# Kernel optimization log

Hardware: AMD Instinct MI355X
Metric: run time of the kernel (lower is better)

Reference implementation:

```python
import jax, jax.numpy as jnp
import numpy as np

N = 50000   # num nodes
E = 400000  # num edges (avg degree 8)
D = 256     # in_channels
H = 256     # hidden_channels
C = 64      # out_channels
K = 2       # k_hops


def setup_inputs() -> dict:
    key = jax.random.key(0)
    ks = jax.random.split(key, 10)
    x = jax.random.normal(ks[0], (N, D), dtype=jnp.float32)
    edge_index = jax.random.randint(ks[1], (2, E), 0, N, dtype=jnp.int32)
    s = 0.05
    # per-hop linears of the single H2GCNConv (weights stored [in, out])
    W0 = jax.random.normal(ks[2], (D, H), jnp.float32) * s
    W1 = jax.random.normal(ks[3], (D, H), jnp.float32) * s
    W2 = jax.random.normal(ks[4], (D, H), jnp.float32) * s
    b0 = jnp.zeros((H,), jnp.float32)
    b1 = jnp.zeros((H,), jnp.float32)
    b2 = jnp.zeros((H,), jnp.float32)
    # classifier: h2_out_dim = H*(K+1) = 768 -> C
    Wc = jax.random.normal(ks[5], (H * (K + 1), C), jnp.float32) * s
    bc = jnp.zeros((C,), jnp.float32)
    return {"x": x, "edge_index": edge_index, "num_nodes": N,
            "W0": W0, "b0": b0, "W1": W1, "b1": b1, "W2": W2, "b2": b2,
            "Wc": Wc, "bc": bc}


def _normalize_adj(edge_index, num_nodes):
    # add self loops, then D^{-1/2} A D^{-1/2} edge weights
    loops = jnp.arange(num_nodes, dtype=edge_index.dtype)
    ei = jnp.concatenate([edge_index, jnp.stack([loops, loops])], axis=1)
    row, col = ei[0], ei[1]
    deg = jax.ops.segment_sum(jnp.ones(row.shape[0], jnp.float32), row,
                              num_segments=num_nodes)
    dis = jnp.where(deg > 0, deg ** -0.5, 0.0)  # inf -> 0 for isolated nodes
    return ei, dis[row] * dis[col]


def _sparse_mm(edge_index, edge_weight, x, num_nodes):
    # gather -> scale -> scatter-add (COO SpMM)
    row, col = edge_index[0], edge_index[1]
    msg = x[col] * edge_weight[:, None]  # [E', F]
    return jax.ops.segment_sum(msg, row, num_segments=num_nodes)


def reference(x, edge_index, num_nodes, W0, b0, W1, b1, W2, b2, Wc, bc):
    ei, ew = _normalize_adj(edge_index, num_nodes)
    # H2GCNConv: ego + k-hop aggregates, each through its own linear, concat
    outs = [x @ W0 + b0]
    cur = x
    for Wk, bk in ((W1, b1), (W2, b2)):
        cur = _sparse_mm(ei, ew, cur, num_nodes)
        outs.append(cur @ Wk + bk)
    h = jax.nn.relu(jnp.concatenate(outs, axis=1))  # [N, 3H]
    # dropout p=0 / eval mode -> identity
    return h @ Wc + bc
```

## Files before the change

### kernel.cpp

```cpp
#include <hip/hip_runtime.h>


#define FD 256
#define CO 64
#define SB 512

using frag_ab = __attribute__((ext_vector_type(8))) short;
using f32x4   = __attribute__((ext_vector_type(4))) float;
typedef unsigned short u16;
typedef unsigned int   u32;

__device__ __forceinline__ u16 f2bf(float f) {
    u32 u = __builtin_bit_cast(u32, f);
    return (u16)((u + 0x7FFFu + ((u >> 16) & 1u)) >> 16);
}
__device__ __forceinline__ float bfl(u32 packed) {
    return __builtin_bit_cast(float, packed << 16);
}
__device__ __forceinline__ float bfh(u32 packed) {
    return __builtin_bit_cast(float, packed & 0xFFFF0000u);
}

__device__ __forceinline__ void gll16(const void* g, void* l) {
    __builtin_amdgcn_global_load_lds(
        (const __attribute__((address_space(1))) u32*)g,
        (__attribute__((address_space(3))) u32*)l, 16, 0, 0);
}

#define BAR()  __builtin_amdgcn_s_barrier()
#define WLG0() asm volatile("s_waitcnt lgkmcnt(0)" ::: "memory")
#define WVM0() asm volatile("s_waitcnt vmcnt(0)" ::: "memory")
#define WVM2() asm volatile("s_waitcnt vmcnt(2)" ::: "memory")

__global__ void zerok(int4* __restrict__ deg4, int4* __restrict__ fill4, int n4) {
    int i = blockIdx.x * blockDim.x + threadIdx.x;
    int4 z = make_int4(0, 0, 0, 0);
    if (i < n4) { deg4[i] = z; fill4[i] = z; }
}
__global__ void count_kernel(const int* __restrict__ ei0, int* deg, int e) {
    int i = blockIdx.x * blockDim.x + threadIdx.x;
    if (i < e) atomicAdd(&deg[ei0[i]], 1);
}
__global__ void scan1(const int* __restrict__ deg, int* __restrict__ rowptr,
                      int* __restrict__ bsum, float* __restrict__ dis, int n) {
    __shared__ int sh[SB];
    int tid = threadIdx.x;
    int i = blockIdx.x * SB + tid;
    int v = (i < n) ? deg[i] + 1 : 0;
    if (i < n) dis[i] = rsqrtf((float)v);
    sh[tid] = v;
    __syncthreads();
    for (int off = 1; off < SB; off <<= 1) {
        int add = (tid >= off) ? sh[tid - off] : 0;
        __syncthreads();
        sh[tid] += add;
        __syncthreads();
    }
    if (i < n) rowptr[i] = sh[tid] - v;
    if (tid == SB - 1) bsum[blockIdx.x] = sh[tid];
}
__global__ void scan2(const int* __restrict__ bsum, int* __restrict__ bscan, int nb) {
    __shared__ int sh[128];
    int tid = threadIdx.x;
    int v = (tid < nb) ? bsum[tid] : 0;
    sh[tid] = v;
    __syncthreads();
    for (int off = 1; off < 128; off <<= 1) {
        int add = (tid >= off) ? sh[tid - off] : 0;
        __syncthreads();
        sh[tid] += add;
        __syncthreads();
    }
    if (tid < nb) bscan[tid] = sh[tid] - v;
    if (tid == nb - 1) bscan[nb] = sh[tid];
}
__global__ void scan3(int* rowptr, const int* __restrict__ bscan, int n, int nb) {
    int i = blockIdx.x * 256 + threadIdx.x;
    if (i < n) rowptr[i] += bscan[i / SB];
    if (i == n) rowptr[n] = bscan[nb];
}
__global__ void fill_kernel(const int* __restrict__ ei, const float* __restrict__ dis,
                            const int* __restrict__ rowptr, int* fill,
                            int2* __restrict__ cw, int e, int n) {
    int i = blockIdx.x * blockDim.x + threadIdx.x;
    if (i >= e + n) return;
    int r, c;
    if (i < e) { r = ei[i]; c = ei[e + i]; }
    else       { r = i - e; c = r; }
    float w = dis[r] * dis[c];
    int pos = rowptr[r] + atomicAdd(&fill[r], 1);
    int2 p; p.x = c; p.y = __float_as_int(w);
    cw[pos] = p;
}

__global__ void prep_kernel(const float* __restrict__ x, u16* __restrict__ xb, int total4, int cb,
                            const float* __restrict__ W0, const float* __restrict__ W1,
                            const float* __restrict__ W2, const float* __restrict__ Wc,
                            u16* __restrict__ WkT, u16* __restrict__ WcT) {
    __shared__ u16 tl[64][65];
    if (blockIdx.x < cb) {
        int i = blockIdx.x * blockDim.x + threadIdx.x;
        if (i < total4) {
            float4 v = ((const float4*)x)[i];
            ushort4 o;
            o.x = f2bf(v.x); o.y = f2bf(v.y); o.z = f2bf(v.z); o.w = f2bf(v.w);
            ((ushort4*)xb)[i] = o;
        }
        return;
    }
    int b = blockIdx.x - cb;
    const float* src; u16* dst; int R, C, r0, c0;
    if (b < 48) {
        int k = b >> 4, t = b & 15;
        src = (k == 0) ? W0 : (k == 1) ? W1 : W2;
        dst = WkT + k * 65536;
        R = 256; C = 256; r0 = (t >> 2) * 64; c0 = (t & 3) * 64;
    } else {
        int t = b - 48;
        src = Wc; dst = WcT;
        R = 768; C = 64; r0 = t * 64; c0 = 0;
    }
    int tid = threadIdx.x;
    int rr = tid >> 4, cc = (tid & 15) * 4;
    #pragma unroll
    for (int it = 0; it < 4; ++it) {
        int r = it * 16 + rr;
        float4 v = *(const float4*)(src + (size_t)(r0 + r) * C + c0 + cc);
        tl[cc + 0][r] = f2bf(v.x); tl[cc + 1][r] = f2bf(v.y);
        tl[cc + 2][r] = f2bf(v.z); tl[cc + 3][r] = f2bf(v.w);
    }
    __syncthreads();
    #pragma unroll
    for (int it = 0; it < 4; ++it) {
        int crow = it * 16 + rr;
        ushort4 o;
        o.x = tl[crow][cc + 0]; o.y = tl[crow][cc + 1];
        o.z = tl[crow][cc + 2]; o.w = tl[crow][cc + 3];
        *(ushort4*)(dst + (size_t)(c0 + crow) * R + r0 + cc) = o;
    }
}

__global__ void spmm_bf16(const int* __restrict__ rowptr, const int2* __restrict__ cw,
                          const u16* __restrict__ xb, u16* __restrict__ outb, int n) {
    int tid = threadIdx.x;
    int lane = tid & 63;
    int row = blockIdx.x * 8 + ((tid >> 6) << 1) + (lane >> 5);
    if (row >= n) return;
    int l32 = lane & 31;
    int p0 = rowptr[row], p1 = rowptr[row + 1];
    float a[8];
    #pragma unroll
    for (int j = 0; j < 8; ++j) a[j] = 0.f;

    for (int p = p0; p < p1; p += 8) {
        int2 cwv[8]; uint4 v[8];
        #pragma unroll
        for (int u = 0; u < 8; ++u) {
            int q = p + u;
            bool ok = q < p1;
            cwv[u] = cw[ok ? q : p0];
            if (!ok) cwv[u].y = 0;
        }
        #pragma unroll
        for (int u = 0; u < 8; ++u)
            v[u] = *(const uint4*)(xb + (size_t)cwv[u].x * FD + l32 * 8);
        #pragma unroll
        for (int u = 0; u < 8; ++u) {
            float wt = __int_as_float(cwv[u].y);
            a[0] += wt * bfl(v[u].x); a[1] += wt * bfh(v[u].x);
            a[2] += wt * bfl(v[u].y); a[3] += wt * bfh(v[u].y);
            a[4] += wt * bfl(v[u].z); a[5] += wt * bfh(v[u].z);
            a[6] += wt * bfl(v[u].w); a[7] += wt * bfh(v[u].w);
        }
    }
    uint4 o;
    o.x = (u32)f2bf(a[0]) | ((u32)f2bf(a[1]) << 16);
    o.y = (u32)f2bf(a[2]) | ((u32)f2bf(a[3]) << 16);
    o.z = (u32)f2bf(a[4]) | ((u32)f2bf(a[5]) << 16);
    o.w = (u32)f2bf(a[6]) | ((u32)f2bf(a[7]) << 16);
    *(uint4*)(outb + (size_t)row * FD + l32 * 8) = o;
}

__launch_bounds__(256, 2)
__global__ void fused_gemm(const u16* __restrict__ xb, const u16* __restrict__ agg1b,
                           const u16* __restrict__ agg2b, const u16* __restrict__ WkT,
                           const float* __restrict__ b0, const float* __restrict__ b1,
                           const float* __restrict__ b2, const u16* __restrict__ WcT,
                           const float* __restrict__ bc, float* __restrict__ out, int n) {
    __shared__ __align__(16) char lds[73728];
    char* Tl = lds + 40960;

    const int tid = threadIdx.x;
    const int w = tid >> 6, l = tid & 63;
    const int l4 = l >> 4, lm = l & 15;
    const int row0 = blockIdx.x * 64;
    const int rr = w * 16 + lm;

    f32x4 oacc[4];
    #pragma unroll
    for (int am = 0; am < 4; ++am) oacc[am] = (f32x4)(0.f);

    for (int seg = 0; seg < 3; ++seg) {
        const u16* inb = (seg == 0) ? xb : (seg == 1) ? agg1b : agg2b;
        const u16* WT  = WkT + (size_t)seg * 65536;
        const float* bk = (seg == 0) ? b0 : (seg == 1) ? b1 : b2;

        auto stageB = [&](int kt, int pb) {
            {
                int L = tid * 16;
                int r = L >> 6, s = (L >> 4) & 3;
                int gr = row0 + r; if (gr > n - 1) gr = n - 1;
                gll16(inb + (size_t)gr * FD + kt * 32 + (s ^ (r & 3)) * 8,
                      lds + pb * 4096 + L);
            }
            #pragma unroll
            for (int i = 0; i < 4; ++i) {
                int L = tid * 16 + i * 4096;
                int j = L >> 6, s = (L >> 4) & 3;
                gll16(WT + (size_t)j * FD + kt * 32 + (s ^ (j & 3)) * 8,
                      lds + 8192 + pb * 16384 + L);
            }
        };

        f32x4 acc[4][4];
        #pragma unroll
        for (int jm = 0; jm < 4; ++jm)
            #pragma unroll
            for (int rn = 0; rn < 4; ++rn) acc[jm][rn] = (f32x4)(0.f);

        stageB(0, 0);
        WVM0();
        BAR();

        #pragma unroll
        for (int kt = 0; kt < 8; ++kt) {
            char* curA = lds + (kt & 1) * 4096;
            char* curW = lds + 8192 + (kt & 1) * 16384;
            if (kt < 7) stageB(kt + 1, (kt + 1) & 1);

            frag_ab af[4], bf_[4];
            #pragma unroll
            for (int jm = 0; jm < 4; ++jm) {
                int j = w * 64 + jm * 16 + lm;
                af[jm] = *(const frag_ab*)(curW + j * 64 + ((l4 ^ (j & 3)) << 4));
            }
            #pragma unroll
            for (int rn = 0; rn < 4; ++rn) {
                int r = rn * 16 + lm;
                bf_[rn] = *(const frag_ab*)(curA + r * 64 + ((l4 ^ (r & 3)) << 4));
            }
            #pragma unroll
            for (int jm = 0; jm < 4; ++jm)
                #pragma unroll
                for (int rn = 0; rn < 4; ++rn)
                    acc[jm][rn] = __builtin_amdgcn_mfma_f32_16x16x32_bf16(af[jm], bf_[rn], acc[jm][rn], 0, 0, 0);

            if (kt < 7) WVM0();
            WLG0();
            BAR();
        }

        auto stageC = [&](int kt2, int pb) {
            #pragma unroll
            for (int i = 0; i < 2; ++i) {
                int L = tid * 16 + i * 4096;
                int c = L >> 7, s = (L >> 4) & 7;
                gll16(WcT + (size_t)c * 768 + seg * 256 + kt2 * 64 + (s ^ (c & 7)) * 8,
                      lds + 8192 + pb * 8192 + L);
            }
        };
        stageC(0, 0);

        #pragma unroll
        for (int jm = 0; jm < 4; ++jm) {
            int j0 = w * 64 + jm * 16 + l4 * 4;
            float4 bb = *(const float4*)(bk + j0);
            #pragma unroll
            for (int rn = 0; rn < 4; ++rn) {
                int r = rn * 16 + lm;
                f32x4 v = acc[jm][rn];
                ushort4 p;
                p.x = f2bf(fmaxf(v[0] + bb.x, 0.f));
                p.y = f2bf(fmaxf(v[1] + bb.y, 0.f));
                p.z = f2bf(fmaxf(v[2] + bb.z, 0.f));
                p.w = f2bf(fmaxf(v[3] + bb.w, 0.f));
                *(ushort4*)(Tl + r * 512 + (((j0 >> 3) ^ (r & 7)) << 4) + (j0 & 7) * 2) = p;
            }
        }
        WLG0();
        BAR();

        #pragma unroll
        for (int kt2 = 0; kt2 < 4; ++kt2) {
            char* cw_ = lds + 8192 + (kt2 & 1) * 8192;
            if (kt2 < 3) {
                stageC(kt2 + 1, (kt2 + 1) & 1);
                WVM2();
            } else {
                WVM0();
            }
            BAR();
            #pragma unroll
            for (int kk2 = 0; kk2 < 2; ++kk2) {
                int g = kt2 * 8 + kk2 * 4 + l4;
                frag_ab bfr = *(const frag_ab*)(Tl + rr * 512 + ((g ^ (rr & 7)) << 4));
                #pragma unroll
                for (int am = 0; am < 4; ++am) {
                    int c = am * 16 + lm;
                    frag_ab afr = *(const frag_ab*)(cw_ + c * 128 + (((kk2 * 4 + l4) ^ (c & 7)) << 4));
                    oacc[am] = __builtin_amdgcn_mfma_f32_16x16x32_bf16(afr, bfr, oacc[am], 0, 0, 0);
                }
            }
            WLG0();
            BAR();
        }
    }

    int gr = row0 + rr;
    if (gr < n) {
        #pragma unroll
        for (int am = 0; am < 4; ++am) {
            float4 bb = *(const float4*)(bc + am * 16 + l4 * 4);
            float4 o;
            o.x = oacc[am][0] + bb.x;
            o.y = oacc[am][1] + bb.y;
            o.z = oacc[am][2] + bb.z;
            o.w = oacc[am][3] + bb.w;
            *(float4*)(out + (size_t)gr * CO + am * 16 + l4 * 4) = o;
        }
    }
}

extern "C" void kernel_launch(void* const* d_in, const int* in_sizes, int n_in,
                              void* d_out, int out_size, void* d_ws, size_t ws_size,
                              hipStream_t stream) {
    const float* x  = (const float*)d_in[0];
    const int*   ei = (const int*)d_in[1];
    const float* W0 = (const float*)d_in[3];
    const float* b0 = (const float*)d_in[4];
    const float* W1 = (const float*)d_in[5];
    const float* b1 = (const float*)d_in[6];
    const float* W2 = (const float*)d_in[7];
    const float* b2 = (const float*)d_in[8];
    const float* Wc = (const float*)d_in[9];
    const float* bc = (const float*)d_in[10];
    float* out = (float*)d_out;

    const int n  = in_sizes[0] / FD;
    const int e  = in_sizes[1] / 2;
    const int ep = e + n;
    const int nb = (n + SB - 1) / SB;

    char* ws = (char*)d_ws;
    size_t o = 0;
    auto take = [&](size_t nbytes) -> char* {
        char* p = ws + o;
        o += (nbytes + 255) & ~(size_t)255;
        return p;
    };
    int*   deg    = (int*)  take((size_t)n * 4);
    int*   fill   = (int*)  take((size_t)n * 4);
    float* dis    = (float*)take((size_t)n * 4);
    int*   rowptr = (int*)  take((size_t)(n + 1) * 4);
    int*   bsum   = (int*)  take((size_t)(nb + 1) * 4);
    int*   bscan  = (int*)  take((size_t)(nb + 1) * 4);
    int2*  cw     = (int2*) take((size_t)ep * 8);
    u16*   xb     = (u16*)  take((size_t)n * FD * 2);
    u16*   agg1b  = (u16*)  take((size_t)n * FD * 2);
    u16*   agg2b  = (u16*)  take((size_t)n * FD * 2);
    u16*   WkT    = (u16*)  take((size_t)3 * FD * FD * 2);
    u16*   WcT    = (u16*)  take((size_t)CO * 3 * FD * 2);
    (void)ws_size; (void)n_in; (void)out_size;

    const int n4 = (n + 3) / 4;
    zerok       <<<(n4 + 255) / 256, 256, 0, stream>>>((int4*)deg, (int4*)fill, n4);
    count_kernel<<<(e + 255) / 256, 256, 0, stream>>>(ei, deg, e);
    scan1       <<<nb, SB, 0, stream>>>(deg, rowptr, bsum, dis, n);
    scan2       <<<1, 128, 0, stream>>>(bsum, bscan, nb);
    scan3       <<<(n + 256) / 256, 256, 0, stream>>>(rowptr, bscan, n, nb);
    fill_kernel <<<(ep + 255) / 256, 256, 0, stream>>>(ei, dis, rowptr, fill, cw, e, n);

    const int total4 = n * FD / 4;
    const int cb = (total4 + 255) / 256;
    prep_kernel<<<cb + 60, 256, 0, stream>>>(x, xb, total4, cb, W0, W1, W2, Wc, WkT, WcT);

    spmm_bf16<<<(n + 7) / 8, 256, 0, stream>>>(rowptr, cw, xb, agg1b, n);
    spmm_bf16<<<(n + 7) / 8, 256, 0, stream>>>(rowptr, cw, agg1b, agg2b, n);

    fused_gemm<<<(n + 63) / 64, 256, 0, stream>>>(xb, agg1b, agg2b, WkT,
                                                  b0, b1, b2, WcT, bc, out, n);
}
```

Baseline: 193.4 us.

## Stage full A tile once and give each wave private W buffers in fused GEMM

The fused GEMM now loads the whole 64x256 input tile into LDS once per segment and gives each wave its own double-buffered slice of the per-hop weight. The k-loop then needs only per-wave vmcnt waits instead of a block-wide barrier every step. The classifier weight slice for each segment is loaded in one piece into the freed A region rather than in four pipelined chunks. LDS use drops from 72KB to 64KB, at the cost of a larger up-front load per segment that is not overlapped with compute.

After: 194.7 us. No clear change (+0.7%).

```diff
diff --git a/kernel.cpp b/kernel.cpp
--- a/kernel.cpp
+++ b/kernel.cpp
@@ -30,7 +30,7 @@
 #define BAR()  __builtin_amdgcn_s_barrier()
 #define WLG0() asm volatile("s_waitcnt lgkmcnt(0)" ::: "memory")
 #define WVM0() asm volatile("s_waitcnt vmcnt(0)" ::: "memory")
-#define WVM2() asm volatile("s_waitcnt vmcnt(2)" ::: "memory")
+#define WVM4() asm volatile("s_waitcnt vmcnt(4)" ::: "memory")
 
 __global__ void zerok(int4* __restrict__ deg4, int4* __restrict__ fill4, int n4) {
     int i = blockIdx.x * blockDim.x + threadIdx.x;
@@ -187,90 +187,95 @@
                            const float* __restrict__ b0, const float* __restrict__ b1,
                            const float* __restrict__ b2, const u16* __restrict__ WcT,
                            const float* __restrict__ bc, float* __restrict__ out, int n) {
-    __shared__ __align__(16) char lds[73728];
-    char* Tl = lds + 40960;
+    __shared__ __align__(16) char lds[65536];
+    char* RA = lds;
+    char* RW = lds + 32768;
 
     const int tid = threadIdx.x;
     const int w = tid >> 6, l = tid & 63;
     const int l4 = l >> 4, lm = l & 15;
     const int row0 = blockIdx.x * 64;
     const int rr = w * 16 + lm;
+    char* myW = RW + w * 8192;
+
+    auto stageA = [&](const u16* inb) {
+        #pragma unroll
+        for (int i = 0; i < 8; ++i) {
+            int L = tid * 16 + i * 4096;
+            int r = L >> 9, g = (L >> 4) & 31;
+            int gr = row0 + r; if (gr > n - 1) gr = n - 1;
+            gll16(inb + (size_t)gr * FD + (g ^ (r & 7)) * 8, RA + L);
+        }
+    };
+    auto stageW = [&](const u16* WT, int kt, int pb) {
+        #pragma unroll
+        for (int i = 0; i < 4; ++i) {
+            int L = l * 16 + i * 1024;
+            int jq = L >> 6, s = (L >> 4) & 3;
+            int j = w * 64 + jq;
+            gll16(WT + (size_t)j * FD + kt * 32 + (s ^ (j & 3)) * 8,
+                  myW + pb * 4096 + L);
+        }
+    };
+    auto stageWc = [&](int seg) {
+        #pragma unroll
+        for (int i = 0; i < 8; ++i) {
+            int L = tid * 16 + i * 4096;
+            int c = L >> 9, g = (L >> 4) & 31;
+            gll16(WcT + (size_t)c * 768 + seg * 256 + (g ^ (c & 7)) * 8, RA + L);
+        }
+    };
 
     f32x4 oacc[4];
     #pragma unroll
     for (int am = 0; am < 4; ++am) oacc[am] = (f32x4)(0.f);
 
+    stageA(xb);
+    stageW(WkT, 0, 0);
+    WVM0();
+    BAR();
+
     for (int seg = 0; seg < 3; ++seg) {
-        const u16* inb = (seg == 0) ? xb : (seg == 1) ? agg1b : agg2b;
-        const u16* WT  = WkT + (size_t)seg * 65536;
+        const u16* WT = WkT + (size_t)seg * 65536;
         const float* bk = (seg == 0) ? b0 : (seg == 1) ? b1 : b2;
 
-        auto stageB = [&](int kt, int pb) {
-            {
-                int L = tid * 16;
-                int r = L >> 6, s = (L >> 4) & 3;
-                int gr = row0 + r; if (gr > n - 1) gr = n - 1;
-                gll16(inb + (size_t)gr * FD + kt * 32 + (s ^ (r & 3)) * 8,
-                      lds + pb * 4096 + L);
-            }
-            #pragma unroll
-            for (int i = 0; i < 4; ++i) {
-                int L = tid * 16 + i * 4096;
-                int j = L >> 6, s = (L >> 4) & 3;
-                gll16(WT + (size_t)j * FD + kt * 32 + (s ^ (j & 3)) * 8,
-                      lds + 8192 + pb * 16384 + L);
-            }
-        };
-
         f32x4 acc[4][4];
         #pragma unroll
         for (int jm = 0; jm < 4; ++jm)
             #pragma unroll
             for (int rn = 0; rn < 4; ++rn) acc[jm][rn] = (f32x4)(0.f);
 
-        stageB(0, 0);
-        WVM0();
-        BAR();
-
         #pragma unroll
         for (int kt = 0; kt < 8; ++kt) {
-            char* curA = lds + (kt & 1) * 4096;
-            char* curW = lds + 8192 + (kt & 1) * 16384;
-            if (kt < 7) stageB(kt + 1, (kt + 1) & 1);
+            if (kt < 7) stageW(WT, kt + 1, (kt + 1) & 1);
+            if (kt == 7)      { WVM0(); }
+            else if (kt > 0)  { WVM4(); }
+            char* curW = myW + (kt & 1) * 4096;
 
             frag_ab af[4], bf_[4];
             #pragma unroll
             for (int jm = 0; jm < 4; ++jm) {
-                int j = w * 64 + jm * 16 + lm;
-                af[jm] = *(const frag_ab*)(curW + j * 64 + ((l4 ^ (j & 3)) << 4));
+                int jq = jm * 16 + lm;
+                int j  = w * 64 + jq;
+                af[jm] = *(const frag_ab*)(curW + jq * 64 + ((l4 ^ (j & 3)) << 4));
             }
             #pragma unroll
             for (int rn = 0; rn < 4; ++rn) {
                 int r = rn * 16 + lm;
-                bf_[rn] = *(const frag_ab*)(curA + r * 64 + ((l4 ^ (r & 3)) << 4));
+                bf_[rn] = *(const frag_ab*)(RA + r * 512 + (((kt * 4 + l4) ^ (r & 7)) << 4));
             }
             #pragma unroll
             for (int jm = 0; jm < 4; ++jm)
                 #pragma unroll
                 for (int rn = 0; rn < 4; ++rn)
                     acc[jm][rn] = __builtin_amdgcn_mfma_f32_16x16x32_bf16(af[jm], bf_[rn], acc[jm][rn], 0, 0, 0);
-
-            if (kt < 7) WVM0();
-            WLG0();
-            BAR();
-        }
-
-        auto stageC = [&](int kt2, int pb) {
-            #pragma unroll
-            for (int i = 0; i < 2; ++i) {
-                int L = tid * 16 + i * 4096;
-                int c = L >> 7, s = (L >> 4) & 7;
-                gll16(WcT + (size_t)c * 768 + seg * 256 + kt2 * 64 + (s ^ (c & 7)) * 8,
-                      lds + 8192 + pb * 8192 + L);
-            }
-        };
-        stageC(0, 0);
-
+        }
+        WLG0();
+        BAR();
+
+        stageWc(seg);
+
+        char* Tl = RW;
         #pragma unroll
         for (int jm = 0; jm < 4; ++jm) {
             int j0 = w * 64 + jm * 16 + l4 * 4;
@@ -287,31 +292,27 @@
                 *(ushort4*)(Tl + r * 512 + (((j0 >> 3) ^ (r & 7)) << 4) + (j0 & 7) * 2) = p;
             }
         }
+        WVM0();
         WLG0();
         BAR();
 
         #pragma unroll
-        for (int kt2 = 0; kt2 < 4; ++kt2) {
-            char* cw_ = lds + 8192 + (kt2 & 1) * 8192;
-            if (kt2 < 3) {
-                stageC(kt2 + 1, (kt2 + 1) & 1);
-                WVM2();
-            } else {
-                WVM0();
+        for (int ks = 0; ks < 8; ++ks) {
+            frag_ab tb = *(const frag_ab*)(Tl + rr * 512 + (((ks * 4 + l4) ^ (rr & 7)) << 4));
+            #pragma unroll
+            for (int am = 0; am < 4; ++am) {
+                int c = am * 16 + lm;
+                frag_ab afr = *(const frag_ab*)(RA + c * 512 + (((ks * 4 + l4) ^ (c & 7)) << 4));
+                oacc[am] = __builtin_amdgcn_mfma_f32_16x16x32_bf16(afr, tb, oacc[am], 0, 0, 0);
             }
-            BAR();
-            #pragma unroll
-            for (int kk2 = 0; kk2 < 2; ++kk2) {
-                int g = kt2 * 8 + kk2 * 4 + l4;
-                frag_ab bfr = *(const frag_ab*)(Tl + rr * 512 + ((g ^ (rr & 7)) << 4));
-                #pragma unroll
-                for (int am = 0; am < 4; ++am) {
-                    int c = am * 16 + lm;
-                    frag_ab afr = *(const frag_ab*)(cw_ + c * 128 + (((kk2 * 4 + l4) ^ (c & 7)) << 4));
-                    oacc[am] = __builtin_amdgcn_mfma_f32_16x16x32_bf16(afr, bfr, oacc[am], 0, 0, 0);
-                }
-            }
-            WLG0();
+        }
+        WLG0();
+        BAR();
+
+        if (seg < 2) {
+            stageA((seg == 0) ? agg1b : agg2b);
+            stageW(WkT + (size_t)(seg + 1) * 65536, 0, 0);
+            WVM0();
             BAR();
         }
     }
```
